# Kernel tuning notes

Hardware: AMD Instinct MI355X
Metric: run time of the kernel (lower is better)

Reference implementation:

```python
import jax, jax.numpy as jnp
import numpy as np

B, S, E, H = 2, 2048, 1024, 16
D = E // H  # head_dim
SCALE = 1.0 / np.sqrt(D)


def rope_tables(seq_len, dim, dtype=jnp.float32):
    # matches RotaryEmbedding: inv_freq over even indices, emb = cat([freqs, freqs])
    inv_freq = 1.0 / (10000.0 ** (jnp.arange(0, dim, 2, dtype=dtype) / dim))
    t = jnp.arange(seq_len, dtype=dtype)
    freqs = t[:, None] * inv_freq[None, :]          # [S, D/2]
    emb = jnp.concatenate([freqs, freqs], axis=-1)  # [S, D]
    return jnp.cos(emb)[None, None], jnp.sin(emb)[None, None]  # [1,1,S,D]


def apply_rope(x, cos, sin):
    # x: [B,H,S,D]; interleaved rotate exactly as the torch code:
    # x2 = stack([-x[...,1::2], x[...,0::2]], -1).reshape_as(x)
    x2 = jnp.stack([-x[..., 1::2], x[..., 0::2]], axis=-1).reshape(x.shape)
    return x * cos + x2 * sin


def setup_inputs() -> dict:
    key = jax.random.key(0)
    ks = jax.random.split(key, 12)
    std = 1.0 / np.sqrt(E)
    inp = {
        "query": jax.random.normal(ks[0], (B, S, E), jnp.float32),
        "key": jax.random.normal(ks[1], (B, S, E), jnp.float32),
        "value": jax.random.normal(ks[2], (B, S, E), jnp.float32),
        "mask": jnp.ones((B, S), jnp.int32),
        "Wq": jax.random.normal(ks[3], (E, E), jnp.float32) * std,
        "bq": jax.random.normal(ks[4], (E,), jnp.float32) * std,
        "Wk": jax.random.normal(ks[5], (E, E), jnp.float32) * std,
        "bk": jax.random.normal(ks[6], (E,), jnp.float32) * std,
        "Wv": jax.random.normal(ks[7], (E, E), jnp.float32) * std,
        "bv": jax.random.normal(ks[8], (E,), jnp.float32) * std,
        "Wo": jax.random.normal(ks[9], (E, E), jnp.float32) * std,
        "bo": jax.random.normal(ks[10], (E,), jnp.float32) * std,
    }
    return inp


def reference(query, key, value, mask, Wq, bq, Wk, bk, Wv, bv, Wo, bo):
    b, sq, _ = query.shape
    sk = key.shape[1]
    # linear projections (torch Linear: x @ W.T + b), split into heads [B,H,S,D]
    Q = (query @ Wq.T + bq).reshape(b, sq, H, D).transpose(0, 2, 1, 3)
    K = (key @ Wk.T + bk).reshape(b, sk, H, D).transpose(0, 2, 1, 3)
    V = (value @ Wv.T + bv).reshape(b, sk, H, D).transpose(0, 2, 1, 3)
    cos_q, sin_q = rope_tables(sq, D)
    cos_k, sin_k = rope_tables(sk, D)
    Q = apply_rope(Q, cos_q, sin_q)
    K = apply_rope(K, cos_k, sin_k)
    scores = jnp.einsum("bhqd,bhkd->bhqk", Q, K) * SCALE
    neg_inf = jnp.finfo(scores.dtype).min
    scores = jnp.where(mask[:, None, None, :] == 0, neg_inf, scores)
    attn = jax.nn.softmax(scores, axis=-1)
    # dropout omitted (deterministic reference / eval mode)
    out = jnp.einsum("bhqk,bhkd->bhqd", attn, V)
    out = out.transpose(0, 2, 1, 3).reshape(b, sq, E)
    return out @ Wo.T + bo
```

## Files before the change

kernel.cpp:

```cpp
#include <hip/hip_runtime.h>
#include <stdint.h>

typedef unsigned short u16;
typedef __bf16 bf16x8 __attribute__((ext_vector_type(8)));
typedef float f32x4 __attribute__((ext_vector_type(4)));
typedef float f32x2 __attribute__((ext_vector_type(2)));
typedef u16 u16x4v __attribute__((ext_vector_type(4)));

#define DI __device__ __forceinline__

constexpr int BB = 2, SS = 2048, EE = 1024, HH = 16, DD = 64;
constexpr int MROWS = BB * SS;
constexpr int KDIM = 1024, NDIM = 1024;

constexpr float FM = 12.0f;
constexpr float MNEG = -30000.f;

DI u16 f2bf(float f) {
  uint32_t u = __float_as_uint(f);
  return (u16)((u + 0x7FFFu + ((u >> 16) & 1u)) >> 16);
}
DI float bf2f(u16 h) { return __uint_as_float(((uint32_t)h) << 16); }

DI uint32_t cvtpk_bf16(float a, float b) {
  uint32_t r;
  asm("v_cvt_pk_bf16_f32 %0, %1, %2" : "=v"(r) : "v"(a), "v"(b));
  return r;
}

DI void cp16(const void* g, void* lds) {
  __builtin_amdgcn_global_load_lds((const __attribute__((address_space(1))) void*)g,
                                   (__attribute__((address_space(3))) void*)lds, 16, 0, 0);
}

DI f32x4 mfma16(bf16x8 a, bf16x8 b, f32x4 c) {
  return __builtin_amdgcn_mfma_f32_16x16x32_bf16(a, b, c, 0, 0, 0);
}

__global__ __launch_bounds__(256) void prep_cast(
    const float* __restrict__ q, const float* __restrict__ k, const float* __restrict__ v,
    const float* __restrict__ wq, const float* __restrict__ wk, const float* __restrict__ wv,
    const float* __restrict__ wo,
    u16* __restrict__ qb, u16* __restrict__ kb, u16* __restrict__ vb,
    u16* __restrict__ wqb, u16* __restrict__ wkb, u16* __restrict__ wvb,
    u16* __restrict__ wob) {
  constexpr size_t SZI = (size_t)MROWS * EE;
  constexpr size_t SZW = (size_t)EE * EE;
  const size_t g = ((size_t)blockIdx.x * 256 + threadIdx.x) * 4;
  const float* src; u16* dst; size_t o;
  if (g < SZI)          { src = q; dst = qb; o = g; }
  else if (g < 2 * SZI) { src = k; dst = kb; o = g - SZI; }
  else if (g < 3 * SZI) { src = v; dst = vb; o = g - 2 * SZI; }
  else {
    size_t t2 = g - 3 * SZI;
    int wi = (int)(t2 / SZW);
    o = t2 - (size_t)(wi < 4 ? wi : 3) * SZW;
    src = wi == 0 ? wq : wi == 1 ? wk : wi == 2 ? wv : wo;
    dst = wi == 0 ? wqb : wi == 1 ? wkb : wi == 2 ? wvb : wob;
  }
  const float4 f = *(const float4*)(src + o);
  u16x4v hv;
  hv[0] = f2bf(f.x); hv[1] = f2bf(f.y); hv[2] = f2bf(f.z); hv[3] = f2bf(f.w);
  *(u16x4v*)(dst + o) = hv;
}

__global__ __launch_bounds__(256) void rope_tables_k(float* __restrict__ csT,
                                                     const int* __restrict__ mask,
                                                     float* __restrict__ mfl) {
  const int t = blockIdx.x * 256 + threadIdx.x;
  const int s = t >> 6, d = t & 63, j = d & 31;
  const float ang = (float)s * exp2f(-(float)j * 0.4152410118f);
  float2 cs; cs.x = cosf(ang); cs.y = sinf(ang);
  ((float2*)csT)[t] = cs;
  if (t < BB * SS) mfl[t] = mask[t] ? -FM : MNEG;
}

__global__ __launch_bounds__(256) void gemm_qkv(
    const u16* __restrict__ qb, const u16* __restrict__ kb, const u16* __restrict__ vb,
    const u16* __restrict__ wqb, const u16* __restrict__ wkb, const u16* __restrict__ wvb,
    const float* __restrict__ bq, const float* __restrict__ bk, const float* __restrict__ bv,
    u16* __restrict__ Qp, u16* __restrict__ Kp, u16* __restrict__ Vtg,
    const float* __restrict__ csT) {
  __shared__ alignas(16) u16 sA[2][128 * 64];
  __shared__ alignas(16) u16 sB[2][128 * 64];
  const int flat = blockIdx.y * 8 + blockIdx.x;
  const int swz = (flat & 7) * 96 + (flat >> 3);
  const int bx = swz & 7, by = swz >> 3;

  const int tsel = by >> 5;
  const bool vtr = (tsel == 2);
  const u16* A    = tsel == 0 ? wqb : tsel == 1 ? wkb : vb;
  const u16* Bm   = tsel == 0 ? qb  : tsel == 1 ? kb  : wvb;
  const float* bias = tsel == 0 ? bq : tsel == 1 ? bk : bv;

  const int fBase = bx * 128;
  const int tBase = (by & 31) * 128;
  const int aBase = vtr ? tBase : fBase;
  const int bBase = vtr ? fBase : tBase;
  const int tid = threadIdx.x;
  const int lane = tid & 63, w = tid >> 6;
  const int quad = lane >> 4, l16 = lane & 15;
  const int wr = w >> 1, wc = w & 1;

  size_t aSrc[4], bSrc[4];
  int dOff[4];
#pragma unroll
  for (int j = 0; j < 4; ++j) {
    const int c = tid + j * 256;
    const int row = c >> 3, sl = c & 7;
    const size_t off = (size_t)row * KDIM + ((sl ^ (row & 7)) * 8);
    aSrc[j] = (size_t)aBase * KDIM + off;
    bSrc[j] = (size_t)bBase * KDIM + off;
    dOff[j] = c * 8;
  }

  f32x4 acc[4][4];
#pragma unroll
  for (int mi = 0; mi < 4; ++mi)
#pragma unroll
    for (int ni = 0; ni < 4; ++ni)
#pragma unroll
      for (int e = 0; e < 4; ++e) acc[mi][ni][e] = 0.f;

  const int arow = wr * 64 + l16, brow = wc * 64 + l16;

  auto stage = [&](int k0, int bi) {
#pragma unroll
    for (int j = 0; j < 4; ++j) {
      cp16(A + aSrc[j] + k0, &sA[bi][dOff[j]]);
      cp16(Bm + bSrc[j] + k0, &sB[bi][dOff[j]]);
    }
  };

  stage(0, 0);
  __syncthreads();
  int buf = 0;
  for (int k0 = 0; k0 < KDIM; k0 += 64) {
    if (k0 + 64 < KDIM) stage(k0 + 64, buf ^ 1);
    __builtin_amdgcn_s_setprio(1);
#pragma unroll
    for (int h = 0; h < 2; ++h) {
      bf16x8 af[4], bf[4];
#pragma unroll
      for (int i = 0; i < 4; ++i) {
        const int ar = arow + i * 16, br = brow + i * 16;
        af[i] = *(const bf16x8*)&sA[buf][ar * 64 + (((h * 4 + quad) ^ (ar & 7)) << 3)];
        bf[i] = *(const bf16x8*)&sB[buf][br * 64 + (((h * 4 + quad) ^ (br & 7)) << 3)];
      }
#pragma unroll
      for (int mi = 0; mi < 4; ++mi)
#pragma unroll
        for (int ni = 0; ni < 4; ++ni)
          acc[mi][ni] = mfma16(af[mi], bf[ni], acc[mi][ni]);
    }
    __builtin_amdgcn_s_setprio(0);
    __syncthreads();
    buf ^= 1;
  }

  if (!vtr) {
    u16* C = tsel == 0 ? Qp : Kp;
#pragma unroll
    for (int mi = 0; mi < 4; ++mi) {
      const int fm = fBase + wr * 64 + mi * 16 + quad * 4;
      const float4 b4 = *(const float4*)&bias[fm];
      const int d0 = fm & 63;
#pragma unroll
      for (int ni = 0; ni < 4; ++ni) {
        const int t = tBase + wc * 64 + ni * 16 + l16;
        const int srow = t & (SS - 1);
        const float* cs = &csT[(size_t)((srow << 6) + d0) * 2];
        const float4 cs01 = *(const float4*)cs;
        const float4 cs23 = *(const float4*)(cs + 4);
        const float v0 = acc[mi][ni][0] + b4.x;
        const float v1 = acc[mi][ni][1] + b4.y;
        const float v2 = acc[mi][ni][2] + b4.z;
        const float v3 = acc[mi][ni][3] + b4.w;
        const float o0 = v0 * cs01.x - v1 * cs01.y;
        const float o1 = v1 * cs01.z + v0 * cs01.w;
        const float o2 = v2 * cs23.x - v3 * cs23.y;
        const float o3 = v3 * cs23.z + v2 * cs23.w;
        uint2 pk;
        pk.x = cvtpk_bf16(o0, o1);
        pk.y = cvtpk_bf16(o2, o3);
        *(uint2*)&C[(size_t)t * NDIM + fm] = pk;
      }
    }
  } else {
#pragma unroll
    for (int ni = 0; ni < 4; ++ni) {
      const int f = fBase + wc * 64 + ni * 16 + l16;
      const int h = f >> 6, d = f & 63;
      const float bb = bias[f];
#pragma unroll
      for (int mi = 0; mi < 4; ++mi) {
        const int t0 = tBase + wr * 64 + mi * 16 + quad * 4;
        const int b = t0 >> 11, s0 = t0 & (SS - 1);
        const int sp0 = (s0 & ~31) | (((s0 >> 2) & 3) << 3) | (((s0 >> 4) & 1) << 2);
        uint2 pk;
        pk.x = cvtpk_bf16(acc[mi][ni][0] + bb, acc[mi][ni][1] + bb);
        pk.y = cvtpk_bf16(acc[mi][ni][2] + bb, acc[mi][ni][3] + bb);
        *(uint2*)&Vtg[((size_t)((b * 16 + h) * 64 + d)) * SS + sp0] = pk;
      }
    }
  }
}

__global__ __launch_bounds__(512, 4) void attn_kernel(
    const u16* __restrict__ Qp, const u16* __restrict__ Kp, const u16* __restrict__ Vtg,
    const float* __restrict__ mfl, u16* __restrict__ Oh) {
  __shared__ alignas(16) u16 sm[36864];
  const int flat = blockIdx.y * 16 + blockIdx.x;
  const int swz = (flat & 7) * 64 + (flat >> 3);
  const int bqx = swz & 15, bh = swz >> 4;

  const int tid = threadIdx.x, lane = tid & 63, w = tid >> 6;
  const int quad = lane >> 4, l16 = lane & 15;
  const int b = bh >> 4, h = bh & 15;
  const int q0 = bqx * 128 + (w & 3) * 32;
  const int grp = w >> 2, wl = w & 3;
  const u16* Qb = Qp + (size_t)b * SS * EE + h * DD;
  const u16* Kb = Kp + (size_t)b * SS * EE + h * DD;
  const u16* Vb = Vtg + (size_t)bh * DD * SS;
  constexpr float C1 = 0.18033688011112042f;
  float* smask = (float*)&sm[32768];

  bf16x8 qf[2][2];
#pragma unroll
  for (int qi = 0; qi < 2; ++qi)
#pragma unroll
    for (int ks = 0; ks < 2; ++ks)
      qf[qi][ks] = *(const bf16x8*)(Qb + (size_t)(q0 + qi * 16 + l16) * EE + ks * 32 + quad * 8);

  f32x4 oacc[2][4];
#pragma unroll
  for (int qi = 0; qi < 2; ++qi)
#pragma unroll
    for (int nd = 0; nd < 4; ++nd)
#pragma unroll
      for (int e = 0; e < 4; ++e) oacc[qi][nd][e] = 0.f;
  f32x2 sum2[2];
  sum2[0] = {0.f, 0.f}; sum2[1] = {0.f, 0.f};

  const int gtid = tid & 255;

  auto stage = [&](int w_, int bi) {
    const int key0 = w_ * 128 + grp * 64;
    u16* dK = &sm[grp * 16384 + bi * 4096];
    u16* dV = &sm[grp * 16384 + 8192 + bi * 4096];
#pragma unroll
    for (int i = 0; i < 2; ++i) {
      const int c = i * 256 + gtid;
      const int key = c >> 3, sl = c & 7;
      cp16(Kb + (size_t)(key0 + key) * EE + ((sl ^ (key & 7)) * 8), &dK[c * 8]);
    }
#pragma unroll
    for (int i = 0; i < 2; ++i) {
      const int c = i * 256 + gtid;
      const int d = c >> 3, sl = c & 7;
      cp16(Vb + (size_t)d * SS + key0 + ((sl ^ (d & 7)) * 8), &dV[c * 8]);
    }
  };

  auto compute = [&](int w_, int bi) {
    const int key0 = w_ * 128 + grp * 64;
    const u16* sK_ = &sm[grp * 16384 + bi * 4096];
    const u16* sV_ = &sm[grp * 16384 + 8192 + bi * 4096];
    f32x4 sacc[2][4];
#pragma unroll
    for (int qi = 0; qi < 2; ++qi)
#pragma unroll
      for (int ni = 0; ni < 4; ++ni)
#pragma unroll
        for (int e = 0; e < 4; ++e) sacc[qi][ni][e] = 0.f;
    __builtin_amdgcn_s_setprio(1);
#pragma unroll
    for (int ks = 0; ks < 2; ++ks)
#pragma unroll
      for (int ni = 0; ni < 4; ++ni) {
        const int row = ni * 16 + l16;
        const bf16x8 kf = *(const bf16x8*)&sK_[row * 64 + (((ks * 4 + quad) ^ (l16 & 7)) << 3)];
#pragma unroll
        for (int qi = 0; qi < 2; ++qi)
          sacc[qi][ni] = mfma16(kf, qf[qi][ks], sacc[qi][ni]);
      }
    __builtin_amdgcn_s_setprio(0);

    uint32_t pw32[2][2][4];
#pragma unroll
    for (int qi = 0; qi < 2; ++qi)
#pragma unroll
      for (int ni = 0; ni < 4; ++ni) {
        const int kb4 = key0 + ni * 16 + quad * 4;
        const f32x2 m01 = *(const f32x2*)&smask[kb4];
        const f32x2 m23 = *(const f32x2*)&smask[kb4 + 2];
        f32x2 t01, t23;
        t01.x = sacc[qi][ni][0]; t01.y = sacc[qi][ni][1];
        t23.x = sacc[qi][ni][2]; t23.y = sacc[qi][ni][3];
        t01 = t01 * C1 + m01;
        t23 = t23 * C1 + m23;
        f32x2 p01, p23;
        p01.x = __builtin_amdgcn_exp2f(t01.x); p01.y = __builtin_amdgcn_exp2f(t01.y);
        p23.x = __builtin_amdgcn_exp2f(t23.x); p23.y = __builtin_amdgcn_exp2f(t23.y);
        sum2[qi] += p01;
        sum2[qi] += p23;
        const int k2 = ni >> 1, j2 = (ni & 1) * 2;
        pw32[qi][k2][j2]     = cvtpk_bf16(p01.x, p01.y);
        pw32[qi][k2][j2 + 1] = cvtpk_bf16(p23.x, p23.y);
      }

    __builtin_amdgcn_s_setprio(1);
#pragma unroll
    for (int k2 = 0; k2 < 2; ++k2) {
      union { uint32_t u[4]; bf16x8 v; } pf[2];
#pragma unroll
      for (int qi = 0; qi < 2; ++qi)
#pragma unroll
        for (int j = 0; j < 4; ++j) pf[qi].u[j] = pw32[qi][k2][j];
#pragma unroll
      for (int nd = 0; nd < 4; ++nd) {
        const int row = nd * 16 + l16;
        const bf16x8 vf = *(const bf16x8*)&sV_[row * 64 + (((k2 * 4 + quad) ^ (l16 & 7)) << 3)];
#pragma unroll
        for (int qi = 0; qi < 2; ++qi)
          oacc[qi][nd] = mfma16(pf[qi].v, vf, oacc[qi][nd]);
      }
    }
    __builtin_amdgcn_s_setprio(0);
  };

  stage(0, 0);
  cp16(mfl + (size_t)b * SS + tid * 4, &sm[32768 + tid * 8]);
  __syncthreads();

  for (int w_ = 0; w_ < 16; ++w_) {
    if (w_ + 1 < 16) stage(w_ + 1, (w_ + 1) & 1);
    compute(w_, w_ & 1);
    __syncthreads();
  }

  float lg[2];
#pragma unroll
  for (int qi = 0; qi < 2; ++qi) {
    float s = sum2[qi].x + sum2[qi].y;
    s += __shfl_xor(s, 16, 64);
    s += __shfl_xor(s, 32, 64);
    lg[qi] = s;
  }

  float* sO = (float*)&sm[0];
  float* l0 = smask;
  if (grp == 0) {
#pragma unroll
    for (int qi = 0; qi < 2; ++qi)
#pragma unroll
      for (int nd = 0; nd < 4; ++nd)
#pragma unroll
        for (int e = 0; e < 4; ++e) {
          const int q = wl * 32 + qi * 16 + quad * 4 + e;
          sO[q * 65 + nd * 16 + l16] = oacc[qi][nd][e];
        }
    if (quad == 0) {
      l0[wl * 32 + l16] = lg[0];
      l0[wl * 32 + 16 + l16] = lg[1];
    }
  }
  __syncthreads();
  if (grp == 1) {
    float linv[2];
#pragma unroll
    for (int qi = 0; qi < 2; ++qi) {
      const float lt = l0[wl * 32 + qi * 16 + l16] + lg[qi];
      linv[qi] = lt > 0.f ? 1.0f / lt : 0.f;
    }
#pragma unroll
    for (int qi = 0; qi < 2; ++qi)
#pragma unroll
      for (int r = 0; r < 4; ++r) {
        const float li = __shfl(linv[qi], quad * 4 + r, 16);
        const int q = wl * 32 + qi * 16 + quad * 4 + r;
        const size_t row = (size_t)(b * SS + bqx * 128 + q) * EE + h * DD;
#pragma unroll
        for (int nd = 0; nd < 4; ++nd) {
          const int d = nd * 16 + l16;
          Oh[row + d] = f2bf((sO[q * 65 + d] + oacc[qi][nd][r]) * li);
        }
      }
  }
}

__global__ __launch_bounds__(256) void gemm_out(
    const u16* __restrict__ Ab, const u16* __restrict__ Bb,
    const float* __restrict__ bias, float* __restrict__ Cout) {
  __shared__ alignas(16) u16 sA[2][128 * 64];
  __shared__ alignas(16) u16 sB[2][64 * 64];
  const int flat = blockIdx.y * 16 + blockIdx.x;
  const int swz = (flat & 7) * 64 + (flat >> 3);
  const int bx = swz & 15, by = swz >> 4;

  const int rowBase = by * 128;
  const int colBase = bx * 64;
  const int tid = threadIdx.x;
  const int lane = tid & 63, w = tid >> 6;
  const int quad = lane >> 4, l16 = lane & 15;
  const int wr = w >> 1, wc = w & 1;

  size_t aSrc[4]; int aOff[4];
  size_t bSrc[2]; int bOff[2];
#pragma unroll
  for (int j = 0; j < 4; ++j) {
    const int c = tid + j * 256;
    const int row = c >> 3, sl = c & 7;
    aSrc[j] = (size_t)(rowBase + row) * KDIM + ((sl ^ (row & 7)) * 8);
    aOff[j] = c * 8;
  }
#pragma unroll
  for (int j = 0; j < 2; ++j) {
    const int c = tid + j * 256;
    const int row = c >> 3, sl = c & 7;
    bSrc[j] = (size_t)(colBase + row) * KDIM + ((sl ^ (row & 7)) * 8);
    bOff[j] = c * 8;
  }

  f32x4 acc[4][2];
#pragma unroll
  for (int mi = 0; mi < 4; ++mi)
#pragma unroll
    for (int ni = 0; ni < 2; ++ni)
#pragma unroll
      for (int e = 0; e < 4; ++e) acc[mi][ni][e] = 0.f;

  const int arow = wr * 64 + l16, brow = wc * 32 + l16;

  auto stage = [&](int k0, int bi) {
#pragma unroll
    for (int j = 0; j < 4; ++j) cp16(Ab + aSrc[j] + k0, &sA[bi][aOff[j]]);
#pragma unroll
    for (int j = 0; j < 2; ++j) cp16(Bb + bSrc[j] + k0, &sB[bi][bOff[j]]);
  };

  stage(0, 0);
  __syncthreads();
  int buf = 0;
  for (int k0 = 0; k0 < KDIM; k0 += 64) {
    if (k0 + 64 < KDIM) stage(k0 + 64, buf ^ 1);
    __builtin_amdgcn_s_setprio(1);
#pragma unroll
    for (int h = 0; h < 2; ++h) {
      bf16x8 af[4], bf[2];
#pragma unroll
      for (int i = 0; i < 4; ++i) {
        const int ar = arow + i * 16;
        af[i] = *(const bf16x8*)&sA[buf][ar * 64 + (((h * 4 + quad) ^ (ar & 7)) << 3)];
      }
#pragma unroll
      for (int i = 0; i < 2; ++i) {
        const int br = brow + i * 16;
        bf[i] = *(const bf16x8*)&sB[buf][br * 64 + (((h * 4 + quad) ^ (br & 7)) << 3)];
      }
#pragma unroll
      for (int mi = 0; mi < 4; ++mi)
#pragma unroll
        for (int ni = 0; ni < 2; ++ni)
          acc[mi][ni] = mfma16(af[mi], bf[ni], acc[mi][ni]);
    }
    __builtin_amdgcn_s_setprio(0);
    __syncthreads();
    buf ^= 1;
  }

#pragma unroll
  for (int mi = 0; mi < 4; ++mi) {
    const int rb = rowBase + wr * 64 + mi * 16 + quad * 4;
#pragma unroll
    for (int ni = 0; ni < 2; ++ni) {
      const int col = colBase + wc * 32 + ni * 16 + l16;
      const float bb = bias[col];
#pragma unroll
      for (int r = 0; r < 4; ++r)
        Cout[(size_t)(rb + r) * NDIM + col] = acc[mi][ni][r] + bb;
    }
  }
}

extern "C" void kernel_launch(void* const* d_in, const int* in_sizes, int n_in,
                              void* d_out, int out_size, void* d_ws, size_t ws_size,
                              hipStream_t stream) {
  const float* q    = (const float*)d_in[0];
  const float* k    = (const float*)d_in[1];
  const float* v    = (const float*)d_in[2];
  const int*   mask = (const int*)d_in[3];
  const float* Wq = (const float*)d_in[4];
  const float* bq = (const float*)d_in[5];
  const float* Wk = (const float*)d_in[6];
  const float* bk = (const float*)d_in[7];
  const float* Wv = (const float*)d_in[8];
  const float* bv = (const float*)d_in[9];
  const float* Wo = (const float*)d_in[10];
  const float* bo = (const float*)d_in[11];
  float* out = (float*)d_out;
  char* ws = (char*)d_ws;
  constexpr size_t MB = 1024 * 1024;
  u16* qb  = (u16*)(ws + 0 * MB);
  u16* kb  = (u16*)(ws + 8 * MB);
  u16* vb  = (u16*)(ws + 16 * MB);
  u16* wqb = (u16*)(ws + 24 * MB);
  u16* wkb = (u16*)(ws + 26 * MB);
  u16* wvb = (u16*)(ws + 28 * MB);
  u16* wob = (u16*)(ws + 30 * MB);
  u16* Qp  = (u16*)(ws + 32 * MB);
  u16* Kp  = (u16*)(ws + 40 * MB);
  u16* Vtg = (u16*)(ws + 48 * MB);
  u16* oh  = (u16*)(ws + 56 * MB);
  float* csT = (float*)(ws + 64 * MB);
  float* mfl = out;

  prep_cast<<<16384, 256, 0, stream>>>(q, k, v, Wq, Wk, Wv, Wo,
                                       qb, kb, vb, wqb, wkb, wvb, wob);
  rope_tables_k<<<512, 256, 0, stream>>>(csT, mask, mfl);
  gemm_qkv<<<dim3(8, 96), 256, 0, stream>>>(qb, kb, vb, wqb, wkb, wvb,
                                            bq, bk, bv, Qp, Kp, Vtg, csT);
  attn_kernel<<<dim3(16, 32), 512, 0, stream>>>(Qp, Kp, Vtg, mfl, oh);
  gemm_out<<<dim3(16, 32), 256, 0, stream>>>(oh, wob, bo, out);
}
```

Measured before the change: 217.7 us.

## Split attention key dimension across four wave groups with 1024-thread blocks

The attention kernel now launches 1024 threads per block, split into four wave groups. Each group handles a 32-key slice of every 128-key window instead of two groups handling 64-key slices. The V tile layout and swizzle are changed to match 32-key rows. Partial outputs and row sums are merged by a two-level tree reduction through shared memory before normalisation and store. This raises the number of waves in flight to hide latency, at the cost of smaller MFMA work per wave, extra barriers, and a longer reduction epilogue.

```diff
diff --git a/kernel.cpp b/kernel.cpp
--- a/kernel.cpp
+++ b/kernel.cpp
@@ -206,7 +206,7 @@
   }
 }
 
-__global__ __launch_bounds__(512, 4) void attn_kernel(
+__global__ __launch_bounds__(1024, 4) void attn_kernel(
     const u16* __restrict__ Qp, const u16* __restrict__ Kp, const u16* __restrict__ Vtg,
     const float* __restrict__ mfl, u16* __restrict__ Oh) {
   __shared__ alignas(16) u16 sm[36864];
@@ -216,9 +216,9 @@
 
   const int tid = threadIdx.x, lane = tid & 63, w = tid >> 6;
   const int quad = lane >> 4, l16 = lane & 15;
+  const int grp = w >> 2, wl = w & 3;
   const int b = bh >> 4, h = bh & 15;
-  const int q0 = bqx * 128 + (w & 3) * 32;
-  const int grp = w >> 2, wl = w & 3;
+  const int q0 = bqx * 128 + wl * 32;
   const u16* Qb = Qp + (size_t)b * SS * EE + h * DD;
   const u16* Kb = Kp + (size_t)b * SS * EE + h * DD;
   const u16* Vb = Vtg + (size_t)bh * DD * SS;
@@ -245,39 +245,35 @@
   const int gtid = tid & 255;
 
   auto stage = [&](int w_, int bi) {
-    const int key0 = w_ * 128 + grp * 64;
-    u16* dK = &sm[grp * 16384 + bi * 4096];
-    u16* dV = &sm[grp * 16384 + 8192 + bi * 4096];
-#pragma unroll
-    for (int i = 0; i < 2; ++i) {
-      const int c = i * 256 + gtid;
-      const int key = c >> 3, sl = c & 7;
-      cp16(Kb + (size_t)(key0 + key) * EE + ((sl ^ (key & 7)) * 8), &dK[c * 8]);
-    }
-#pragma unroll
-    for (int i = 0; i < 2; ++i) {
-      const int c = i * 256 + gtid;
-      const int d = c >> 3, sl = c & 7;
-      cp16(Vb + (size_t)d * SS + key0 + ((sl ^ (d & 7)) * 8), &dV[c * 8]);
+    const int key0 = w_ * 128 + grp * 32;
+    u16* dK = &sm[grp * 8192 + bi * 2048];
+    u16* dV = &sm[grp * 8192 + 4096 + bi * 2048];
+    {
+      const int key = gtid >> 3, sl = gtid & 7;
+      cp16(Kb + (size_t)(key0 + key) * EE + ((sl ^ (key & 7)) * 8), &dK[gtid * 8]);
+    }
+    {
+      const int d = gtid >> 2, sl = gtid & 3;
+      cp16(Vb + (size_t)d * SS + key0 + ((sl ^ ((d >> 1) & 3)) * 8), &dV[gtid * 8]);
     }
   };
 
   auto compute = [&](int w_, int bi) {
-    const int key0 = w_ * 128 + grp * 64;
-    const u16* sK_ = &sm[grp * 16384 + bi * 4096];
-    const u16* sV_ = &sm[grp * 16384 + 8192 + bi * 4096];
-    f32x4 sacc[2][4];
-#pragma unroll
-    for (int qi = 0; qi < 2; ++qi)
-#pragma unroll
-      for (int ni = 0; ni < 4; ++ni)
+    const int key0 = w_ * 128 + grp * 32;
+    const u16* sK_ = &sm[grp * 8192 + bi * 2048];
+    const u16* sV_ = &sm[grp * 8192 + 4096 + bi * 2048];
+    f32x4 sacc[2][2];
+#pragma unroll
+    for (int qi = 0; qi < 2; ++qi)
+#pragma unroll
+      for (int ni = 0; ni < 2; ++ni)
 #pragma unroll
         for (int e = 0; e < 4; ++e) sacc[qi][ni][e] = 0.f;
     __builtin_amdgcn_s_setprio(1);
 #pragma unroll
     for (int ks = 0; ks < 2; ++ks)
 #pragma unroll
-      for (int ni = 0; ni < 4; ++ni) {
+      for (int ni = 0; ni < 2; ++ni) {
         const int row = ni * 16 + l16;
         const bf16x8 kf = *(const bf16x8*)&sK_[row * 64 + (((ks * 4 + quad) ^ (l16 & 7)) << 3)];
 #pragma unroll
@@ -286,11 +282,11 @@
       }
     __builtin_amdgcn_s_setprio(0);
 
-    uint32_t pw32[2][2][4];
-#pragma unroll
-    for (int qi = 0; qi < 2; ++qi)
-#pragma unroll
-      for (int ni = 0; ni < 4; ++ni) {
+    uint32_t pw32[2][4];
+#pragma unroll
+    for (int qi = 0; qi < 2; ++qi)
+#pragma unroll
+      for (int ni = 0; ni < 2; ++ni) {
         const int kb4 = key0 + ni * 16 + quad * 4;
         const f32x2 m01 = *(const f32x2*)&smask[kb4];
         const f32x2 m23 = *(const f32x2*)&smask[kb4 + 2];
@@ -304,33 +300,29 @@
         p23.x = __builtin_amdgcn_exp2f(t23.x); p23.y = __builtin_amdgcn_exp2f(t23.y);
         sum2[qi] += p01;
         sum2[qi] += p23;
-        const int k2 = ni >> 1, j2 = (ni & 1) * 2;
-        pw32[qi][k2][j2]     = cvtpk_bf16(p01.x, p01.y);
-        pw32[qi][k2][j2 + 1] = cvtpk_bf16(p23.x, p23.y);
+        pw32[qi][ni * 2]     = cvtpk_bf16(p01.x, p01.y);
+        pw32[qi][ni * 2 + 1] = cvtpk_bf16(p23.x, p23.y);
       }
 
     __builtin_amdgcn_s_setprio(1);
-#pragma unroll
-    for (int k2 = 0; k2 < 2; ++k2) {
-      union { uint32_t u[4]; bf16x8 v; } pf[2];
+    union { uint32_t u[4]; bf16x8 v; } pf[2];
+#pragma unroll
+    for (int qi = 0; qi < 2; ++qi)
+#pragma unroll
+      for (int j = 0; j < 4; ++j) pf[qi].u[j] = pw32[qi][j];
+#pragma unroll
+    for (int nd = 0; nd < 4; ++nd) {
+      const int row = nd * 16 + l16;
+      const bf16x8 vf = *(const bf16x8*)&sV_[row * 32 + ((quad ^ ((row >> 1) & 3)) << 3)];
 #pragma unroll
       for (int qi = 0; qi < 2; ++qi)
-#pragma unroll
-        for (int j = 0; j < 4; ++j) pf[qi].u[j] = pw32[qi][k2][j];
-#pragma unroll
-      for (int nd = 0; nd < 4; ++nd) {
-        const int row = nd * 16 + l16;
-        const bf16x8 vf = *(const bf16x8*)&sV_[row * 64 + (((k2 * 4 + quad) ^ (l16 & 7)) << 3)];
-#pragma unroll
-        for (int qi = 0; qi < 2; ++qi)
-          oacc[qi][nd] = mfma16(pf[qi].v, vf, oacc[qi][nd]);
-      }
+        oacc[qi][nd] = mfma16(pf[qi].v, vf, oacc[qi][nd]);
     }
     __builtin_amdgcn_s_setprio(0);
   };
 
   stage(0, 0);
-  cp16(mfl + (size_t)b * SS + tid * 4, &sm[32768 + tid * 8]);
+  if (tid < 512) cp16(mfl + (size_t)b * SS + tid * 4, &sm[32768 + tid * 8]);
   __syncthreads();
 
   for (int w_ = 0; w_ < 16; ++w_) {
@@ -349,41 +341,84 @@
   }
 
   float* sO = (float*)&sm[0];
-  float* l0 = smask;
-  if (grp == 0) {
+  float* lf = smask;
+  if (grp >= 2) {
+    const int r = (grp - 2) * 4 + wl;
 #pragma unroll
     for (int qi = 0; qi < 2; ++qi)
 #pragma unroll
       for (int nd = 0; nd < 4; ++nd)
 #pragma unroll
         for (int e = 0; e < 4; ++e) {
-          const int q = wl * 32 + qi * 16 + quad * 4 + e;
-          sO[q * 65 + nd * 16 + l16] = oacc[qi][nd][e];
+          const int q = qi * 16 + quad * 4 + e;
+          const int d = nd * 16 + l16;
+          sO[r * 2048 + q * 64 + (d ^ ((q & 12) << 1))] = oacc[qi][nd][e];
         }
     if (quad == 0) {
-      l0[wl * 32 + l16] = lg[0];
-      l0[wl * 32 + 16 + l16] = lg[1];
-    }
+      lf[(grp - 2) * 128 + wl * 32 + l16]      = lg[0];
+      lf[(grp - 2) * 128 + wl * 32 + 16 + l16] = lg[1];
+    }
+  }
+  __syncthreads();
+  if (grp < 2) {
+    const int r = grp * 4 + wl;
+#pragma unroll
+    for (int qi = 0; qi < 2; ++qi)
+#pragma unroll
+      for (int nd = 0; nd < 4; ++nd)
+#pragma unroll
+        for (int e = 0; e < 4; ++e) {
+          const int q = qi * 16 + quad * 4 + e;
+          const int d = nd * 16 + l16;
+          oacc[qi][nd][e] += sO[r * 2048 + q * 64 + (d ^ ((q & 12) << 1))];
+        }
+    lg[0] += lf[grp * 128 + wl * 32 + l16];
+    lg[1] += lf[grp * 128 + wl * 32 + 16 + l16];
   }
   __syncthreads();
   if (grp == 1) {
+#pragma unroll
+    for (int qi = 0; qi < 2; ++qi)
+#pragma unroll
+      for (int nd = 0; nd < 4; ++nd)
+#pragma unroll
+        for (int e = 0; e < 4; ++e) {
+          const int q = qi * 16 + quad * 4 + e;
+          const int d = nd * 16 + l16;
+          sO[wl * 2048 + q * 64 + (d ^ ((q & 12) << 1))] = oacc[qi][nd][e];
+        }
+    if (quad == 0) {
+      lf[256 + wl * 32 + l16]      = lg[0];
+      lf[256 + wl * 32 + 16 + l16] = lg[1];
+    }
+  }
+  __syncthreads();
+  if (grp == 0) {
+#pragma unroll
+    for (int qi = 0; qi < 2; ++qi)
+#pragma unroll
+      for (int nd = 0; nd < 4; ++nd)
+#pragma unroll
+        for (int e = 0; e < 4; ++e) {
+          const int q = qi * 16 + quad * 4 + e;
+          const int d = nd * 16 + l16;
+          oacc[qi][nd][e] += sO[wl * 2048 + q * 64 + (d ^ ((q & 12) << 1))];
+        }
+    lg[0] += lf[256 + wl * 32 + l16];
+    lg[1] += lf[256 + wl * 32 + 16 + l16];
     float linv[2];
-#pragma unroll
-    for (int qi = 0; qi < 2; ++qi) {
-      const float lt = l0[wl * 32 + qi * 16 + l16] + lg[qi];
-      linv[qi] = lt > 0.f ? 1.0f / lt : 0.f;
-    }
-#pragma unroll
-    for (int qi = 0; qi < 2; ++qi)
-#pragma unroll
-      for (int r = 0; r < 4; ++r) {
-        const float li = __shfl(linv[qi], quad * 4 + r, 16);
-        const int q = wl * 32 + qi * 16 + quad * 4 + r;
-        const size_t row = (size_t)(b * SS + bqx * 128 + q) * EE + h * DD;
+    linv[0] = lg[0] > 0.f ? 1.0f / lg[0] : 0.f;
+    linv[1] = lg[1] > 0.f ? 1.0f / lg[1] : 0.f;
+#pragma unroll
+    for (int qi = 0; qi < 2; ++qi)
+#pragma unroll
+      for (int r4 = 0; r4 < 4; ++r4) {
+        const float li = __shfl(linv[qi], quad * 4 + r4, 16);
+        const size_t row = (size_t)(b * SS + q0 + qi * 16 + quad * 4 + r4) * EE + h * DD;
 #pragma unroll
         for (int nd = 0; nd < 4; ++nd) {
           const int d = nd * 16 + l16;
-          Oh[row + d] = f2bf((sO[q * 65 + d] + oacc[qi][nd][r]) * li);
+          Oh[row + d] = f2bf(oacc[qi][nd][r4] * li);
         }
       }
   }
@@ -520,6 +555,6 @@
   rope_tables_k<<<512, 256, 0, stream>>>(csT, mask, mfl);
   gemm_qkv<<<dim3(8, 96), 256, 0, stream>>>(qb, kb, vb, wqb, wkb, wvb,
                                             bq, bk, bv, Qp, Kp, Vtg, csT);
-  attn_kernel<<<dim3(16, 32), 512, 0, stream>>>(Qp, Kp, Vtg, mfl, oh);
+  attn_kernel<<<dim3(16, 32), 1024, 0, stream>>>(Qp, Kp, Vtg, mfl, oh);
   gemm_out<<<dim3(16, 32), 256, 0, stream>>>(oh, wob, bo, out);
 }
```

Result: slower. 226.7 us (+4.1%).

## Fold rope table kernel into cast kernel; single-buffer QKV GEMM for occupancy

Applied to the files above, without the earlier changes.

The rope cos/sin table and mask-fill work moves into the prep_cast kernel, which removes one kernel launch. The QKV GEMM drops from double-buffered to single-buffered LDS (32KB instead of 64KB) and adds a launch_bounds minimum of 4 blocks per SM, so more workgroups can be resident. The cost is that global-to-LDS loads no longer overlap with MFMA compute inside a workgroup, and there are two barriers per k-step. The bet is that overlap between co-resident workgroups makes up for that.

```diff
diff --git a/kernel.cpp b/kernel.cpp
--- a/kernel.cpp
+++ b/kernel.cpp
@@ -40,12 +40,20 @@
 __global__ __launch_bounds__(256) void prep_cast(
     const float* __restrict__ q, const float* __restrict__ k, const float* __restrict__ v,
     const float* __restrict__ wq, const float* __restrict__ wk, const float* __restrict__ wv,
-    const float* __restrict__ wo,
+    const float* __restrict__ wo, const int* __restrict__ mask,
     u16* __restrict__ qb, u16* __restrict__ kb, u16* __restrict__ vb,
     u16* __restrict__ wqb, u16* __restrict__ wkb, u16* __restrict__ wvb,
-    u16* __restrict__ wob) {
+    u16* __restrict__ wob, float* __restrict__ csT, float* __restrict__ mfl) {
   constexpr size_t SZI = (size_t)MROWS * EE;
   constexpr size_t SZW = (size_t)EE * EE;
+  const int t = blockIdx.x * 256 + threadIdx.x;
+  if (t < SS * 64) {
+    const int s = t >> 6, d = t & 63, j = d & 31;
+    const float ang = (float)s * exp2f(-(float)j * 0.4152410118f);
+    float2 cs; cs.x = cosf(ang); cs.y = sinf(ang);
+    ((float2*)csT)[t] = cs;
+    if (t < BB * SS) mfl[t] = mask[t] ? -FM : MNEG;
+  }
   const size_t g = ((size_t)blockIdx.x * 256 + threadIdx.x) * 4;
   const float* src; u16* dst; size_t o;
   if (g < SZI)          { src = q; dst = qb; o = g; }
@@ -64,25 +72,14 @@
   *(u16x4v*)(dst + o) = hv;
 }
 
-__global__ __launch_bounds__(256) void rope_tables_k(float* __restrict__ csT,
-                                                     const int* __restrict__ mask,
-                                                     float* __restrict__ mfl) {
-  const int t = blockIdx.x * 256 + threadIdx.x;
-  const int s = t >> 6, d = t & 63, j = d & 31;
-  const float ang = (float)s * exp2f(-(float)j * 0.4152410118f);
-  float2 cs; cs.x = cosf(ang); cs.y = sinf(ang);
-  ((float2*)csT)[t] = cs;
-  if (t < BB * SS) mfl[t] = mask[t] ? -FM : MNEG;
-}
-
-__global__ __launch_bounds__(256) void gemm_qkv(
+__global__ __launch_bounds__(256, 4) void gemm_qkv(
     const u16* __restrict__ qb, const u16* __restrict__ kb, const u16* __restrict__ vb,
     const u16* __restrict__ wqb, const u16* __restrict__ wkb, const u16* __restrict__ wvb,
     const float* __restrict__ bq, const float* __restrict__ bk, const float* __restrict__ bv,
     u16* __restrict__ Qp, u16* __restrict__ Kp, u16* __restrict__ Vtg,
     const float* __restrict__ csT) {
-  __shared__ alignas(16) u16 sA[2][128 * 64];
-  __shared__ alignas(16) u16 sB[2][128 * 64];
+  __shared__ alignas(16) u16 sA[128 * 64];
+  __shared__ alignas(16) u16 sB[128 * 64];
   const int flat = blockIdx.y * 8 + blockIdx.x;
   const int swz = (flat & 7) * 96 + (flat >> 3);
   const int bx = swz & 7, by = swz >> 3;
@@ -124,19 +121,14 @@
 
   const int arow = wr * 64 + l16, brow = wc * 64 + l16;
 
-  auto stage = [&](int k0, int bi) {
+  for (int k0 = 0; k0 < KDIM; k0 += 64) {
+    __syncthreads();
 #pragma unroll
     for (int j = 0; j < 4; ++j) {
-      cp16(A + aSrc[j] + k0, &sA[bi][dOff[j]]);
-      cp16(Bm + bSrc[j] + k0, &sB[bi][dOff[j]]);
-    }
-  };
-
-  stage(0, 0);
-  __syncthreads();
-  int buf = 0;
-  for (int k0 = 0; k0 < KDIM; k0 += 64) {
-    if (k0 + 64 < KDIM) stage(k0 + 64, buf ^ 1);
+      cp16(A + aSrc[j] + k0, &sA[dOff[j]]);
+      cp16(Bm + bSrc[j] + k0, &sB[dOff[j]]);
+    }
+    __syncthreads();
     __builtin_amdgcn_s_setprio(1);
 #pragma unroll
     for (int h = 0; h < 2; ++h) {
@@ -144,8 +136,8 @@
 #pragma unroll
       for (int i = 0; i < 4; ++i) {
         const int ar = arow + i * 16, br = brow + i * 16;
-        af[i] = *(const bf16x8*)&sA[buf][ar * 64 + (((h * 4 + quad) ^ (ar & 7)) << 3)];
-        bf[i] = *(const bf16x8*)&sB[buf][br * 64 + (((h * 4 + quad) ^ (br & 7)) << 3)];
+        af[i] = *(const bf16x8*)&sA[ar * 64 + (((h * 4 + quad) ^ (ar & 7)) << 3)];
+        bf[i] = *(const bf16x8*)&sB[br * 64 + (((h * 4 + quad) ^ (br & 7)) << 3)];
       }
 #pragma unroll
       for (int mi = 0; mi < 4; ++mi)
@@ -154,8 +146,6 @@
           acc[mi][ni] = mfma16(af[mi], bf[ni], acc[mi][ni]);
     }
     __builtin_amdgcn_s_setprio(0);
-    __syncthreads();
-    buf ^= 1;
   }
 
   if (!vtr) {
@@ -515,9 +505,8 @@
   float* csT = (float*)(ws + 64 * MB);
   float* mfl = out;
 
-  prep_cast<<<16384, 256, 0, stream>>>(q, k, v, Wq, Wk, Wv, Wo,
-                                       qb, kb, vb, wqb, wkb, wvb, wob);
-  rope_tables_k<<<512, 256, 0, stream>>>(csT, mask, mfl);
+  prep_cast<<<16384, 256, 0, stream>>>(q, k, v, Wq, Wk, Wv, Wo, mask,
+                                       qb, kb, vb, wqb, wkb, wvb, wob, csT, mfl);
   gemm_qkv<<<dim3(8, 96), 256, 0, stream>>>(qb, kb, vb, wqb, wkb, wvb,
                                             bq, bk, bv, Qp, Kp, Vtg, csT);
   attn_kernel<<<dim3(16, 32), 512, 0, stream>>>(Qp, Kp, Vtg, mfl, oh);
```

Result: no change. 215.6 us (-0.9%).
